# Optimization experiments

Hardware: AMD Instinct MI355X
Metric: run time of the kernel (lower is better)

## Reference

```python
import jax, jax.numpy as jnp
import numpy as np
import math

B, C, H, WIN = 8, 96, 224, 7
D_STATE, DT_RANK = 16, 6
PERK = C // 4
K_RATIO = 0.25


def nearest_perfect_square(val):
    if val <= 0:
        return 0
    s = math.sqrt(val)
    lo = math.floor(s) ** 2
    hi = math.ceil(s) ** 2
    return lo if abs(lo - val) <= abs(hi - val) else hi


def setup_inputs() -> dict:
    key = jax.random.key(0)
    ks = jax.random.split(key, 8)
    x = jax.random.normal(ks[0], (B, C, H, H), dtype=jnp.float32)
    router_w1 = jax.random.normal(ks[1], (C // 4, C), jnp.float32) * (1.0 / math.sqrt(C))
    router_b1 = jnp.zeros((C // 4,), jnp.float32)
    router_w2 = jax.random.normal(ks[2], (1, C // 4), jnp.float32) * (1.0 / math.sqrt(C // 4))
    router_b2 = jnp.zeros((1,), jnp.float32)
    x_proj_weight = jax.random.normal(ks[3], (4, DT_RANK + 2 * D_STATE, PERK), jnp.float32) * (1.0 / math.sqrt(PERK))
    std = DT_RANK ** -0.5
    dt_projs_weight = jax.random.uniform(ks[4], (4, PERK, DT_RANK), jnp.float32, -std, std)
    dt = jnp.exp(jax.random.uniform(ks[5], (4, PERK), jnp.float32) * (math.log(0.1) - math.log(0.001)) + math.log(0.001))
    dt = jnp.clip(dt, 1e-4)
    dt_projs_bias = dt + jnp.log(-jnp.expm1(-dt))  # inv-softplus init as in dt_init_fn
    A_logs = jnp.log(jnp.tile(jnp.arange(1, D_STATE + 1, dtype=jnp.float32)[None, :], (4 * PERK, 1)))
    Ds = jnp.ones((4 * PERK,), jnp.float32)
    return {"x": x, "router_w1": router_w1, "router_b1": router_b1, "router_w2": router_w2,
            "router_b2": router_b2, "x_proj_weight": x_proj_weight, "dt_projs_weight": dt_projs_weight,
            "dt_projs_bias": dt_projs_bias, "A_logs": A_logs, "Ds": Ds}


def reference(x, router_w1, router_b1, router_w2, router_b2, x_proj_weight,
              dt_projs_weight, dt_projs_bias, A_logs, Ds):
    Bb, Cc, Hh, Ww = x.shape
    nH = Hh // WIN
    N = nH * nH
    # window partition: b c (nh p1) (nw p2) -> b (nh nw) c p1 p2
    windows = x.reshape(Bb, Cc, nH, WIN, nH, WIN).transpose(0, 2, 4, 1, 3, 5).reshape(Bb, N, Cc, WIN, WIN)
    # router scores
    pooled = windows.mean(axis=(-2, -1))  # [B,N,C]
    hid = jax.nn.gelu(pooled @ router_w1.T + router_b1, approximate=False)
    logits = (hid @ router_w2.T + router_b2)[..., 0]  # [B,N]
    probs = jax.nn.softmax(logits, axis=1)
    top_k = min(max(nearest_perfect_square(N * K_RATIO), 1), N)
    n = int(math.isqrt(top_k))
    rw, sel = jax.lax.top_k(probs, top_k)  # sorted descending, like torch.topk
    windows_flat = windows.reshape(Bb, N, -1)
    cur = jnp.take_along_axis(windows_flat, sel[:, :, None], axis=1)  # [B,topk,C*w*w]
    cur = cur.reshape(Bb, n, n, Cc, WIN, WIN)
    L = n * n * WIN * WIN
    # channel interleave (p k) -> (k p), k=4
    x_int = cur.reshape(Bb, n, n, Cc // 4, 4, WIN, WIN).transpose(0, 1, 2, 4, 3, 5, 6)  # [B,n,n,4,perK,w,w]

    def local_scan(w, column_first, flip):
        # w: [B,n,n,D,wh,ww] -> [B,D,L]
        if column_first:
            w = w.transpose(0, 3, 2, 1, 5, 4)
        else:
            w = w.transpose(0, 3, 1, 2, 4, 5)
        w = w.reshape(Bb, -1, L)
        if flip:
            w = w[..., ::-1]
        return w

    xs = jnp.stack([
        local_scan(x_int[:, :, :, 0], False, False),
        local_scan(x_int[:, :, :, 1], True, False),
        local_scan(x_int[:, :, :, 2], False, True),
        local_scan(x_int[:, :, :, 3], True, True),
    ], axis=1)  # [B,4,perK,L]

    x_dbl = jnp.einsum('bkdl,kcd->bkcl', xs, x_proj_weight)
    dts = x_dbl[:, :, :DT_RANK]
    Bmat = x_dbl[:, :, DT_RANK:DT_RANK + D_STATE]  # [B,4,Nst,L]
    Cmat = x_dbl[:, :, DT_RANK + D_STATE:]
    dts = jnp.einsum('bkrl,kdr->bkdl', dts, dt_projs_weight)  # [B,4,perK,L]
    A_g = -jnp.exp(A_logs).reshape(4, PERK, D_STATE)
    delta = jax.nn.softplus(dts + dt_projs_bias.reshape(4, PERK)[None, :, :, None])

    # selective scan (grouped): h_{l} = exp(delta*A)*h_{l-1} + delta*u*B_l ; y_l = <h_l, C_l>
    dl = jnp.moveaxis(delta, -1, 0)  # [L,B,4,perK]
    ul = jnp.moveaxis(xs, -1, 0)
    Bl = jnp.moveaxis(Bmat, -1, 0)   # [L,B,4,Nst]
    Cl = jnp.moveaxis(Cmat, -1, 0)
    h0 = jnp.zeros((Bb, 4, PERK, D_STATE), jnp.float32)

    def step(h, inp):
        d, u, Bt, Ct = inp
        h = jnp.exp(d[..., None] * A_g) * h + (d * u)[..., None] * Bt[:, :, None, :]
        return h, jnp.einsum('bkdn,bkn->bkd', h, Ct)

    _, ys = jax.lax.scan(step, h0, (dl, ul, Bl, Cl))
    y = jnp.moveaxis(ys, 0, -1) + xs * Ds.reshape(4, PERK)[None, :, :, None]  # [B,4,perK,L]

    def local_reverse(yk, column_first, flip):
        if flip:
            yk = yk[..., ::-1]
        if column_first:
            yk = yk.reshape(Bb, -1, n, n, WIN, WIN).transpose(0, 1, 3, 5, 2, 4).reshape(Bb, -1, L)
        else:
            yk = yk.reshape(Bb, -1, n, n, WIN, WIN).transpose(0, 1, 2, 4, 3, 5).reshape(Bb, -1, L)
        return yk

    yout = jnp.concatenate([
        local_reverse(y[:, 0], False, False),
        local_reverse(y[:, 1], True, False),
        local_reverse(y[:, 2], False, True),
        local_reverse(y[:, 3], True, True),
    ], axis=1)  # [B,C,L]
    yout = yout.reshape(Bb, Cc, n * n, WIN * WIN).transpose(0, 2, 1, 3).reshape(Bb, top_k, -1)
    cur_out = yout * rw[:, :, None]
    residual = windows_flat * probs[:, :, None]
    residual = residual.at[jnp.arange(Bb)[:, None], sel].set(cur_out)
    new = windows_flat + residual
    return new.reshape(Bb, Cc, -1)
```

## Files before the change

### kernel.cpp

```cpp
#include <hip/hip_runtime.h>
#include <math.h>

#define BBATCH 8
#define CC 96
#define HH 224
#define NHW 32
#define NWIN 1024
#define TOPK 256
#define PERK 24
#define DST 16
#define DTR 6
#define LL 12544
#define LCP 52
#define NG 13
#define TCH 256
#define NBK 32
#define XROW 1248
#define WST2 2912

#define OFF_POOL 0
#define OFF_LOG  786432
#define OFF_PROB 794624
#define OFF_RW   802816
#define OFF_RANK 804864
#define OFF_SEL  813056
#define OFF_WEFF 815104
#define OFF_CP   820480
#define OFF_CS   3966208
#define OFF_XSD  7111936
#define OFF_STG  17335552

#define ROR_ADD(v, CTRL) \
    v += __int_as_float(__builtin_amdgcn_update_dpp(0, __float_as_int(v), CTRL, 0xf, 0xf, true))

__global__ void k_weff(const float* __restrict__ xpw, const float* __restrict__ dtw,
                       float* __restrict__ wcomb) {
    int i = blockIdx.x * blockDim.x + threadIdx.x;
    if (i >= 4 * 56 * PERK) return;
    int k = i / (56 * PERK), rem = i - k * (56 * PERK);
    int row = rem / PERK, c = rem - row * PERK;
    float v;
    if (row < PERK) {
        v = 0.f;
        #pragma unroll
        for (int r = 0; r < DTR; ++r)
            v += dtw[(k * PERK + row) * DTR + r] * xpw[(k * 38 + r) * PERK + c];
    } else {
        v = xpw[(k * 38 + (row - PERK + DTR)) * PERK + c];
    }
    wcomb[i] = v;
}

__global__ void k_pool(const float* __restrict__ x, float* __restrict__ pooled) {
    int bc = blockIdx.x;
    const float* xp = x + (size_t)bc * HH * HH;
    float* pp = pooled + (size_t)bc * NWIN;
    for (int w = threadIdx.x; w < NWIN; w += blockDim.x) {
        int wr = w >> 5, wc = w & 31;
        const float* base = xp + (wr * 7) * HH + wc * 7;
        float s = 0.f;
        #pragma unroll
        for (int i = 0; i < 7; ++i) {
            #pragma unroll
            for (int j = 0; j < 7; ++j) s += base[i * HH + j];
        }
        pp[w] = s * (1.0f / 49.0f);
    }
}

__global__ __launch_bounds__(64) void k_router(
        const float* __restrict__ pooled,
        const float* __restrict__ w1, const float* __restrict__ b1,
        const float* __restrict__ w2, const float* __restrict__ b2,
        float* __restrict__ logits) {
    __shared__ float sw1[PERK * CC];
    __shared__ float sb1[PERK];
    __shared__ float sw2[PERK];
    int b = blockIdx.x >> 4, slice = blockIdx.x & 15;
    int tid = threadIdx.x;
    for (int i = tid; i < PERK * CC; i += 64) sw1[i] = w1[i];
    if (tid < PERK) { sb1[tid] = b1[tid]; sw2[tid] = w2[tid]; }
    __syncthreads();
    int w = slice * 64 + tid;
    float hid[PERK];
    #pragma unroll
    for (int j = 0; j < PERK; ++j) hid[j] = sb1[j];
    const float* pp = pooled + (size_t)b * CC * NWIN + w;
    for (int c = 0; c < CC; ++c) {
        float pv = pp[(size_t)c * NWIN];
        #pragma unroll
        for (int j = 0; j < PERK; ++j) hid[j] += pv * sw1[j * CC + c];
    }
    float lg = b2[0];
    #pragma unroll
    for (int j = 0; j < PERK; ++j) {
        float hv = hid[j];
        float g = 0.5f * hv * (1.0f + erff(hv * 0.7071067811865476f));
        lg += g * sw2[j];
    }
    logits[b * NWIN + w] = lg;
}

__global__ __launch_bounds__(64) void k_rankF(const float* __restrict__ logits,
        float* __restrict__ probs, float* __restrict__ rw,
        int* __restrict__ rank, int* __restrict__ sel) {
    __shared__ __attribute__((aligned(16))) float sp[NWIN];
    __shared__ float red[64];
    int b = blockIdx.x >> 4, slice = blockIdx.x & 15;
    int tid = threadIdx.x;
    for (int i = tid; i < NWIN / 4; i += 64)
        ((float4*)sp)[i] = ((const float4*)(logits + (size_t)b * NWIN))[i];
    __syncthreads();
    float m = -1e30f;
    for (int i = tid; i < NWIN; i += 64) m = fmaxf(m, sp[i]);
    red[tid] = m; __syncthreads();
    for (int o = 32; o > 0; o >>= 1) { if (tid < o) red[tid] = fmaxf(red[tid], red[tid + o]); __syncthreads(); }
    float mx = red[0]; __syncthreads();
    for (int i = tid; i < NWIN; i += 64) sp[i] = expf(sp[i] - mx);
    __syncthreads();
    float s = 0.f;
    for (int i = tid; i < NWIN; i += 64) s += sp[i];
    red[tid] = s; __syncthreads();
    for (int o = 32; o > 0; o >>= 1) { if (tid < o) red[tid] += red[tid + o]; __syncthreads(); }
    float sum = red[0]; __syncthreads();
    for (int i = tid; i < NWIN; i += 64) sp[i] = sp[i] / sum;
    __syncthreads();
    int w = slice * 64 + tid;
    float p = sp[w];
    probs[b * NWIN + w] = p;
    int r = 0;
    for (int j = 0; j < NWIN; j += 4) {
        float4 pj = *(const float4*)&sp[j];
        r += (int)((pj.x > p) || (pj.x == p && (j + 0) < w));
        r += (int)((pj.y > p) || (pj.y == p && (j + 1) < w));
        r += (int)((pj.z > p) || (pj.z == p && (j + 2) < w));
        r += (int)((pj.w > p) || (pj.w == p && (j + 3) < w));
    }
    rank[b * NWIN + w] = r;
    if (r < TOPK) { sel[b * TOPK + r] = w; rw[b * TOPK + r] = p; }
}

__device__ __forceinline__ float softplus_f(float v) {
    return fmaxf(v, 0.f) + __logf(1.0f + __expf(-fabsf(v)));
}

__device__ __forceinline__ int window_wsel(const int* sel, int b, int k, int t) {
    int qscan = (k >= 2) ? (255 - t) : t;
    int selidx = (k & 1) ? (((qscan & 15) << 4) | (qscan >> 4)) : qscan;
    return sel[b * TOPK + selidx];
}

__global__ __launch_bounds__(256) void k_gather(const float* __restrict__ x,
        const int* __restrict__ sel, float* __restrict__ xsd) {
    const int total = NBK * TCH * XROW;
    for (int e = blockIdx.x * 256 + threadIdx.x; e < total; e += gridDim.x * 256) {
        int blk = e / XROW;
        int rem = e - blk * XROW;
        int d2 = rem / LCP, j = rem - d2 * LCP;
        float v = 0.f;
        if (j < 49) {
            int t = blk & 255, bk = blk >> 8, k = bk & 3, b = bk >> 2;
            int wsel = window_wsel(sel, b, k, t);
            int pix = (k >= 2) ? 48 - j : j;
            int q7 = pix / 7, r7 = pix - q7 * 7;
            int wi = (k & 1) ? r7 : q7;
            int wj = (k & 1) ? q7 : r7;
            v = x[(((size_t)b * CC + 4 * d2 + k) * HH + (wsel >> 5) * 7 + wi) * HH
                  + (wsel & 31) * 7 + wj];
        }
        xsd[e] = v;
    }
}

__global__ __launch_bounds__(384, 4) void k_prodD(
        const float* __restrict__ xsd, const float* __restrict__ wcomb,
        const float* __restrict__ dtb, const float* __restrict__ alogs,
        float* __restrict__ stage, float* __restrict__ carrP, float* __restrict__ carrS) {
    __shared__ __attribute__((aligned(16))) float sxs[PERK][LCP];
    __shared__ __attribute__((aligned(16))) float sprj[56][LCP];
    __shared__ float swt[56 * PERK];
    __shared__ float sbias[PERK];
    int blk = blockIdx.x;
    int bk = blk >> 8; int k = bk & 3;
    int tid = threadIdx.x;
    const float4* xin = (const float4*)(xsd + (size_t)blk * XROW);
    for (int i = tid; i < XROW / 4; i += 384) ((float4*)sxs)[i] = xin[i];
    for (int i = tid; i < 56 * PERK; i += 384) swt[i] = wcomb[k * (56 * PERK) + i];
    if (tid < PERK) sbias[tid] = dtb[k * PERK + tid];
    if (tid < 168) {
        int r = tid / 3, j = 49 + tid % 3;
        sprj[r][j] = 0.f;
    }
    int d = tid >> 4, s = tid & 15;
    float A = -__expf(alogs[(k * PERK + d) * DST + s]);
    __syncthreads();
    for (int idx = tid; idx < 56 * NG; idx += 384) {
        int row = idx / NG, g = idx - row * NG; int j = g * 4;
        float bs = (row < PERK) ? sbias[row] : 0.f;
        float ax = bs, ay = bs, az = bs, aw = bs;
        #pragma unroll
        for (int d2 = 0; d2 < PERK; ++d2) {
            float w = swt[row * PERK + d2];
            float4 v = *(const float4*)&sxs[d2][j];
            ax += w * v.x; ay += w * v.y; az += w * v.z; aw += w * v.w;
        }
        if (row < PERK) {
            ax = softplus_f(ax); ay = softplus_f(ay); az = softplus_f(az); aw = softplus_f(aw);
        }
        float* dst = &sprj[row][j];
        if (g < 12) { float4 o = {ax, ay, az, aw}; *(float4*)dst = o; }
        else dst[0] = ax;
    }
    __syncthreads();
    float4* sg = (float4*)(stage + (size_t)blk * WST2);
    const float4* sp4 = (const float4*)&sprj[0][0];
    for (int i = tid; i < WST2 / 4; i += 384) sg[i] = sp4[i];
    float P = 1.f, S = 0.f;
    for (int g = 0; g < NG; ++g) {
        int j = g * 4;
        float4 dl4 = *(const float4*)&sprj[d][j];
        float4 xs4 = *(const float4*)&sxs[d][j];
        float4 B4  = *(const float4*)&sprj[24 + s][j];
        float aa;
        aa = __expf(dl4.x * A); S = aa * S + (dl4.x * xs4.x) * B4.x; P *= aa;
        aa = __expf(dl4.y * A); S = aa * S + (dl4.y * xs4.y) * B4.y; P *= aa;
        aa = __expf(dl4.z * A); S = aa * S + (dl4.z * xs4.z) * B4.z; P *= aa;
        aa = __expf(dl4.w * A); S = aa * S + (dl4.w * xs4.w) * B4.w; P *= aa;
    }
    size_t cidx = (size_t)blk * 384 + tid;
    carrP[cidx] = P; carrS[cidx] = S;
}

__global__ void k_carry(const float* carrP, const float* carrS, float* hin) {
    int gid = blockIdx.x * blockDim.x + threadIdx.x;
    int bk = gid / 384, ds = gid - bk * 384;
    float Hv = 0.f;
    for (int t = 0; t < TCH; ++t) {
        size_t idx = ((size_t)bk * TCH + t) * 384 + ds;
        float pv = carrP[idx], sv = carrS[idx];
        hin[idx] = Hv;
        Hv = pv * Hv + sv;
    }
}

__global__ __launch_bounds__(64) void k_base(const float* __restrict__ x,
        const float* __restrict__ probs, const int* __restrict__ rank,
        float* __restrict__ out) {
    int wr = blockIdx.x % NHW; int bc = blockIdx.x / NHW;
    int b = bc / CC;
    __shared__ float buf[7 * HH];
    __shared__ float fmul[NHW];
    __shared__ int   fsel[NHW];
    int tid = threadIdx.x;
    const float* xp = x + ((size_t)bc * HH + wr * 7) * HH;
    for (int i = tid; i < 7 * HH; i += 64) buf[i] = xp[i];
    if (tid < NHW) {
        int w = wr * NHW + tid;
        fsel[tid] = (rank[b * NWIN + w] < TOPK);
        fmul[tid] = 1.0f + probs[b * NWIN + w];
    }
    __syncthreads();
    int c = bc - b * CC;
    for (int idx = tid; idx < NHW * 49; idx += 64) {
        int wc = idx / 49, r = idx - wc * 49;
        if (fsel[wc]) continue;
        int ri = r / 7, rj = r - ri * 7;
        float v = buf[ri * HH + wc * 7 + rj];
        int w = wr * NHW + wc;
        out[(((size_t)b * NWIN + w) * CC + c) * 49 + r] = v * fmul[wc];
    }
}

__global__ __launch_bounds__(384, 4) void k_scan2(
        const float* __restrict__ alogs, const float* __restrict__ dsv,
        const float* __restrict__ hin, const float* __restrict__ xsd,
        float* __restrict__ stage) {
    __shared__ __attribute__((aligned(16))) float sy[PERK][LCP];
    int blk = blockIdx.x;
    int bk = blk >> 8; int k = bk & 3;
    int tid = threadIdx.x;
    int d = tid >> 4, s = tid & 15;
    float A = -__expf(alogs[(k * PERK + d) * DST + s]);
    float Dsr = dsv[k * PERK + d];
    size_t cidx = (size_t)blk * 384 + tid;
    float h = hin[cidx];
    const float* sg = stage + (size_t)blk * WST2;
    const float* pdl = sg + d * LCP;
    const float* pB  = sg + (24 + s) * LCP;
    const float* pC  = sg + (40 + s) * LCP;
    const float* pxs = xsd + (size_t)blk * XROW + d * LCP;
    float4 dlC = *(const float4*)(pdl);     float4 xsC = *(const float4*)(pxs);
    float4 BC_ = *(const float4*)(pB);      float4 CC_ = *(const float4*)(pC);
    float4 dlN = *(const float4*)(pdl + 4); float4 xsN = *(const float4*)(pxs + 4);
    float4 BN_ = *(const float4*)(pB + 4);  float4 CN_ = *(const float4*)(pC + 4);
    for (int g = 0; g < NG; ++g) {
        float4 dl4 = dlC, xs4 = xsC, B4 = BC_, C4 = CC_;
        dlC = dlN; xsC = xsN; BC_ = BN_; CC_ = CN_;
        if (g + 2 < NG) {
            int jn = (g + 2) * 4;
            dlN = *(const float4*)(pdl + jn); xsN = *(const float4*)(pxs + jn);
            BN_ = *(const float4*)(pB + jn);  CN_ = *(const float4*)(pC + jn);
        }
        int j = g * 4;
        float aa, part;
        aa = __expf(dl4.x * A); h = aa * h + (dl4.x * xs4.x) * B4.x;
        part = h * C4.x;
        ROR_ADD(part, 0x121); ROR_ADD(part, 0x122); ROR_ADD(part, 0x124); ROR_ADD(part, 0x128);
        if (s == 0) sy[d][j] = part + xs4.x * Dsr;
        aa = __expf(dl4.y * A); h = aa * h + (dl4.y * xs4.y) * B4.y;
        part = h * C4.y;
        ROR_ADD(part, 0x121); ROR_ADD(part, 0x122); ROR_ADD(part, 0x124); ROR_ADD(part, 0x128);
        if (s == 0 && j + 1 < 49) sy[d][j + 1] = part + xs4.y * Dsr;
        aa = __expf(dl4.z * A); h = aa * h + (dl4.z * xs4.z) * B4.z;
        part = h * C4.z;
        ROR_ADD(part, 0x121); ROR_ADD(part, 0x122); ROR_ADD(part, 0x124); ROR_ADD(part, 0x128);
        if (s == 0 && j + 2 < 49) sy[d][j + 2] = part + xs4.z * Dsr;
        aa = __expf(dl4.w * A); h = aa * h + (dl4.w * xs4.w) * B4.w;
        part = h * C4.w;
        ROR_ADD(part, 0x121); ROR_ADD(part, 0x122); ROR_ADD(part, 0x124); ROR_ADD(part, 0x128);
        if (s == 0 && j + 3 < 49) sy[d][j + 3] = part + xs4.w * Dsr;
    }
    __syncthreads();
    float* yout = stage + (size_t)blk * WST2;
    for (int idx = tid; idx < PERK * 49; idx += 384) {
        int j = idx / PERK, d2 = idx - j * PERK;
        yout[idx] = sy[d2][j];
    }
}

__global__ __launch_bounds__(256) void k_yadd(const float* __restrict__ stage,
        const float* __restrict__ x, const int* __restrict__ sel,
        const float* __restrict__ rw, float* __restrict__ out) {
    __shared__ float ytile[CC * 49];
    int qo = blockIdx.x & 255; int b = blockIdx.x >> 8;
    int wsel = sel[b * TOPK + qo];
    float p = rw[b * TOPK + qo];
    for (int idx = threadIdx.x; idx < CC * 49; idx += 256) {
        int k = idx / 1176; int r1 = idx - k * 1176;
        int u = r1 / 168;   int r2 = r1 - u * 168;
        int wj = r2 / 24;   int d = r2 - wj * 24;
        int rest = qo * 7 + u;
        int b2 = rest & 15; int aw = rest >> 4;
        int wi = aw % 7;    int a = aw / 7;
        int q   = (k & 1) ? (b2 * 16 + a) : (a * 16 + b2);
        int pix = (k & 1) ? (wj * 7 + wi) : (wi * 7 + wj);
        int uu = q * 49 + pix;
        int l = (k >= 2) ? (LL - 1 - uu) : uu;
        int bk = b * 4 + k;
        int t2 = l / 49, jj = l - t2 * 49;
        ytile[(k * PERK + d) * 49 + u * 7 + wj] =
            p * stage[((size_t)(bk * 256 + t2)) * WST2 + jj * PERK + d];
    }
    __syncthreads();
    float* ob = out + ((size_t)(b * NWIN + wsel) * CC) * 49;
    int gi0 = (wsel >> 5) * 7, gj0 = (wsel & 31) * 7;
    for (int e = threadIdx.x; e < CC * 49; e += 256) {
        int C = e / 49, cell = e - C * 49;
        int u = cell / 7, wj = cell - u * 7;
        float xv = x[(((size_t)b * CC + C) * HH + gi0 + u) * HH + gj0 + wj];
        ob[e] = xv + ytile[e];
    }
}

extern "C" void kernel_launch(void* const* d_in, const int* in_sizes, int n_in,
                              void* d_out, int out_size, void* d_ws, size_t ws_size,
                              hipStream_t stream) {
    const float* x   = (const float*)d_in[0];
    const float* w1  = (const float*)d_in[1];
    const float* b1  = (const float*)d_in[2];
    const float* w2  = (const float*)d_in[3];
    const float* b2  = (const float*)d_in[4];
    const float* xpw = (const float*)d_in[5];
    const float* dtw = (const float*)d_in[6];
    const float* dtb = (const float*)d_in[7];
    const float* alg = (const float*)d_in[8];
    const float* dsv = (const float*)d_in[9];
    float* out = (float*)d_out;
    float* ws  = (float*)d_ws;

    float* pooled = ws + OFF_POOL;
    float* logits = ws + OFF_LOG;
    float* probs  = ws + OFF_PROB;
    float* rwv    = ws + OFF_RW;
    int*   rank   = (int*)(ws + OFF_RANK);
    int*   sel    = (int*)(ws + OFF_SEL);
    float* wcomb  = ws + OFF_WEFF;
    float* cP  = ws + OFF_CP;
    float* cS  = ws + OFF_CS;
    float* xsd = ws + OFF_XSD;
    float* stage = ws + OFF_STG;

    k_pool  <<<BBATCH * CC, 256, 0, stream>>>(x, pooled);
    k_router<<<BBATCH * 16, 64, 0, stream>>>(pooled, w1, b1, w2, b2, logits);
    k_rankF <<<BBATCH * 16, 64, 0, stream>>>(logits, probs, rwv, rank, sel);
    k_weff  <<<(4 * 56 * PERK + 255) / 256, 256, 0, stream>>>(xpw, dtw, wcomb);
    k_gather<<<2048, 256, 0, stream>>>(x, sel, xsd);
    k_prodD <<<NBK * TCH, 384, 0, stream>>>(xsd, wcomb, dtb, alg, stage, cP, cS);
    k_carry <<<48, 256, 0, stream>>>(cP, cS, cP);
    k_base  <<<BBATCH * CC * NHW, 64, 0, stream>>>(x, probs, rank, out);
    k_scan2 <<<NBK * TCH, 384, 0, stream>>>(alg, dsv, cP, xsd, stage);
    k_yadd  <<<BBATCH * TOPK, 256, 0, stream>>>(stage, x, sel, rwv, out);
}
```

Baseline: 487.8 us.

## Interleave scan staging data into packed float4 records for the scan pass

```diff
diff --git a/kernel.cpp b/kernel.cpp
--- a/kernel.cpp
+++ b/kernel.cpp
@@ -17,6 +17,7 @@
 #define NBK 32
 #define XROW 1248
 #define WST2 2912
+#define WST3 4000
 
 #define OFF_POOL 0
 #define OFF_LOG  786432
@@ -29,6 +30,8 @@
 #define OFF_CS   3966208
 #define OFF_XSD  7111936
 #define OFF_STG  17335552
+#define NEED_T   ((size_t)(17335552 + 8192 * WST3) * 4)
+#define NEED_F   ((size_t)(17335552 + 8192 * WST2) * 4)
 
 #define ROR_ADD(v, CTRL) \
     v += __int_as_float(__builtin_amdgcn_update_dpp(0, __float_as_int(v), CTRL, 0xf, 0xf, true))
@@ -172,27 +175,15 @@
     }
 }
 
-__global__ __launch_bounds__(384, 4) void k_prodD(
-        const float* __restrict__ xsd, const float* __restrict__ wcomb,
-        const float* __restrict__ dtb, const float* __restrict__ alogs,
-        float* __restrict__ stage, float* __restrict__ carrP, float* __restrict__ carrS) {
-    __shared__ __attribute__((aligned(16))) float sxs[PERK][LCP];
-    __shared__ __attribute__((aligned(16))) float sprj[56][LCP];
-    __shared__ float swt[56 * PERK];
-    __shared__ float sbias[PERK];
-    int blk = blockIdx.x;
-    int bk = blk >> 8; int k = bk & 3;
-    int tid = threadIdx.x;
+__device__ __forceinline__ void proj_body(
+        float (*sxs)[LCP], float (*sprj)[LCP], float* swt, float* sbias,
+        const float* xsd, const float* wcomb, const float* dtb,
+        int blk, int k, int tid) {
     const float4* xin = (const float4*)(xsd + (size_t)blk * XROW);
     for (int i = tid; i < XROW / 4; i += 384) ((float4*)sxs)[i] = xin[i];
     for (int i = tid; i < 56 * PERK; i += 384) swt[i] = wcomb[k * (56 * PERK) + i];
     if (tid < PERK) sbias[tid] = dtb[k * PERK + tid];
-    if (tid < 168) {
-        int r = tid / 3, j = 49 + tid % 3;
-        sprj[r][j] = 0.f;
-    }
-    int d = tid >> 4, s = tid & 15;
-    float A = -__expf(alogs[(k * PERK + d) * DST + s]);
+    if (tid < 168) { int r = tid / 3, j = 49 + tid % 3; sprj[r][j] = 0.f; }
     __syncthreads();
     for (int idx = tid; idx < 56 * NG; idx += 384) {
         int row = idx / NG, g = idx - row * NG; int j = g * 4;
@@ -212,9 +203,13 @@
         else dst[0] = ax;
     }
     __syncthreads();
-    float4* sg = (float4*)(stage + (size_t)blk * WST2);
-    const float4* sp4 = (const float4*)&sprj[0][0];
-    for (int i = tid; i < WST2 / 4; i += 384) sg[i] = sp4[i];
+}
+
+__device__ __forceinline__ void carry_body(
+        float (*sxs)[LCP], float (*sprj)[LCP], const float* alogs,
+        int blk, int k, int tid, float* carrP, float* carrS) {
+    int d = tid >> 4, s = tid & 15;
+    float A = -__expf(alogs[(k * PERK + d) * DST + s]);
     float P = 1.f, S = 0.f;
     for (int g = 0; g < NG; ++g) {
         int j = g * 4;
@@ -231,6 +226,51 @@
     carrP[cidx] = P; carrS[cidx] = S;
 }
 
+__global__ __launch_bounds__(384, 4) void k_prodT(
+        const float* __restrict__ xsd, const float* __restrict__ wcomb,
+        const float* __restrict__ dtb, const float* __restrict__ alogs,
+        float* __restrict__ stage, float* __restrict__ carrP, float* __restrict__ carrS) {
+    __shared__ __attribute__((aligned(16))) float sxs[PERK][LCP];
+    __shared__ __attribute__((aligned(16))) float sprj[56][LCP];
+    __shared__ float swt[56 * PERK];
+    __shared__ float sbias[PERK];
+    int blk = blockIdx.x; int k = (blk >> 8) & 3;
+    int tid = threadIdx.x;
+    proj_body(sxs, sprj, swt, sbias, xsd, wcomb, dtb, blk, k, tid);
+    float4* sgP = (float4*)(stage + (size_t)blk * WST3);
+    float4* sgQ = sgP + 600;
+    for (int tsk = tid; tsk < 600; tsk += 384) {
+        int jp = tsk / 24, d2 = tsk - jp * 24;
+        int j0 = 2 * jp, j1 = j0 + 1;
+        float4 o = { sprj[d2][j0], sxs[d2][j0], sprj[d2][j1], sxs[d2][j1] };
+        sgP[tsk] = o;
+    }
+    for (int tsk = tid; tsk < 400; tsk += 384) {
+        int jp = tsk / 16, s2 = tsk - jp * 16;
+        int j0 = 2 * jp, j1 = j0 + 1;
+        float4 o = { sprj[24 + s2][j0], sprj[40 + s2][j0], sprj[24 + s2][j1], sprj[40 + s2][j1] };
+        sgQ[tsk] = o;
+    }
+    carry_body(sxs, sprj, alogs, blk, k, tid, carrP, carrS);
+}
+
+__global__ __launch_bounds__(384, 4) void k_prodD(
+        const float* __restrict__ xsd, const float* __restrict__ wcomb,
+        const float* __restrict__ dtb, const float* __restrict__ alogs,
+        float* __restrict__ stage, float* __restrict__ carrP, float* __restrict__ carrS) {
+    __shared__ __attribute__((aligned(16))) float sxs[PERK][LCP];
+    __shared__ __attribute__((aligned(16))) float sprj[56][LCP];
+    __shared__ float swt[56 * PERK];
+    __shared__ float sbias[PERK];
+    int blk = blockIdx.x; int k = (blk >> 8) & 3;
+    int tid = threadIdx.x;
+    proj_body(sxs, sprj, swt, sbias, xsd, wcomb, dtb, blk, k, tid);
+    float4* sg = (float4*)(stage + (size_t)blk * WST2);
+    const float4* sp4 = (const float4*)&sprj[0][0];
+    for (int i = tid; i < WST2 / 4; i += 384) sg[i] = sp4[i];
+    carry_body(sxs, sprj, alogs, blk, k, tid, carrP, carrS);
+}
+
 __global__ void k_carry(const float* carrP, const float* carrS, float* hin) {
     int gid = blockIdx.x * blockDim.x + threadIdx.x;
     int bk = gid / 384, ds = gid - bk * 384;
@@ -271,13 +311,51 @@
     }
 }
 
+__global__ __launch_bounds__(384, 4) void k_scanT(
+        const float* __restrict__ alogs, const float* __restrict__ dsv,
+        const float* __restrict__ hin, const float* __restrict__ stage,
+        float* __restrict__ xsd) {
+    __shared__ __attribute__((aligned(16))) float sy[PERK][LCP];
+    int blk = blockIdx.x; int k = (blk >> 8) & 3;
+    int tid = threadIdx.x;
+    int d = tid >> 4, s = tid & 15;
+    float A = -__expf(alogs[(k * PERK + d) * DST + s]);
+    float Dsr = dsv[k * PERK + d];
+    size_t cidx = (size_t)blk * 384 + tid;
+    float h = hin[cidx];
+    const float4* pP = (const float4*)(stage + (size_t)blk * WST3) + d;
+    const float4* pQ = (const float4*)(stage + (size_t)blk * WST3) + 600 + s;
+    float4 Pc = pP[0],  Qc = pQ[0];
+    float4 Pn = pP[24], Qn = pQ[16];
+    for (int jp = 0; jp < 25; ++jp) {
+        float4 P4 = Pc, Q4 = Qc;
+        Pc = Pn; Qc = Qn;
+        if (jp + 2 < 25) { Pn = pP[(jp + 2) * 24]; Qn = pQ[(jp + 2) * 16]; }
+        int j0 = 2 * jp;
+        float aa, part;
+        aa = __expf(P4.x * A); h = aa * h + (P4.x * P4.y) * Q4.x;
+        part = h * Q4.y;
+        ROR_ADD(part, 0x121); ROR_ADD(part, 0x122); ROR_ADD(part, 0x124); ROR_ADD(part, 0x128);
+        if (s == 0) sy[d][j0] = part + P4.y * Dsr;
+        aa = __expf(P4.z * A); h = aa * h + (P4.z * P4.w) * Q4.z;
+        part = h * Q4.w;
+        ROR_ADD(part, 0x121); ROR_ADD(part, 0x122); ROR_ADD(part, 0x124); ROR_ADD(part, 0x128);
+        if (s == 0 && j0 + 1 < 49) sy[d][j0 + 1] = part + P4.w * Dsr;
+    }
+    __syncthreads();
+    float* yout = xsd + (size_t)blk * XROW;
+    for (int idx = tid; idx < PERK * 49; idx += 384) {
+        int j = idx / PERK, d2 = idx - j * PERK;
+        yout[idx] = sy[d2][j];
+    }
+}
+
 __global__ __launch_bounds__(384, 4) void k_scan2(
         const float* __restrict__ alogs, const float* __restrict__ dsv,
         const float* __restrict__ hin, const float* __restrict__ xsd,
         float* __restrict__ stage) {
     __shared__ __attribute__((aligned(16))) float sy[PERK][LCP];
-    int blk = blockIdx.x;
-    int bk = blk >> 8; int k = bk & 3;
+    int blk = blockIdx.x; int k = (blk >> 8) & 3;
     int tid = threadIdx.x;
     int d = tid >> 4, s = tid & 15;
     float A = -__expf(alogs[(k * PERK + d) * DST + s]);
@@ -328,9 +406,9 @@
     }
 }
 
-__global__ __launch_bounds__(256) void k_yadd(const float* __restrict__ stage,
+__global__ __launch_bounds__(256) void k_yadd(const float* __restrict__ ysrc,
         const float* __restrict__ x, const int* __restrict__ sel,
-        const float* __restrict__ rw, float* __restrict__ out) {
+        const float* __restrict__ rw, float* __restrict__ out, int ystride) {
     __shared__ float ytile[CC * 49];
     int qo = blockIdx.x & 255; int b = blockIdx.x >> 8;
     int wsel = sel[b * TOPK + qo];
@@ -349,7 +427,7 @@
         int bk = b * 4 + k;
         int t2 = l / 49, jj = l - t2 * 49;
         ytile[(k * PERK + d) * 49 + u * 7 + wj] =
-            p * stage[((size_t)(bk * 256 + t2)) * WST2 + jj * PERK + d];
+            p * ysrc[((size_t)(bk * 256 + t2)) * ystride + jj * PERK + d];
     }
     __syncthreads();
     float* ob = out + ((size_t)(b * NWIN + wsel) * CC) * 49;
@@ -395,9 +473,18 @@
     k_rankF <<<BBATCH * 16, 64, 0, stream>>>(logits, probs, rwv, rank, sel);
     k_weff  <<<(4 * 56 * PERK + 255) / 256, 256, 0, stream>>>(xpw, dtw, wcomb);
     k_gather<<<2048, 256, 0, stream>>>(x, sel, xsd);
-    k_prodD <<<NBK * TCH, 384, 0, stream>>>(xsd, wcomb, dtb, alg, stage, cP, cS);
-    k_carry <<<48, 256, 0, stream>>>(cP, cS, cP);
-    k_base  <<<BBATCH * CC * NHW, 64, 0, stream>>>(x, probs, rank, out);
-    k_scan2 <<<NBK * TCH, 384, 0, stream>>>(alg, dsv, cP, xsd, stage);
-    k_yadd  <<<BBATCH * TOPK, 256, 0, stream>>>(stage, x, sel, rwv, out);
-}
+
+    if (ws_size >= NEED_T) {
+        k_prodT<<<NBK * TCH, 384, 0, stream>>>(xsd, wcomb, dtb, alg, stage, cP, cS);
+        k_carry<<<48, 256, 0, stream>>>(cP, cS, cP);
+        k_base <<<BBATCH * CC * NHW, 64, 0, stream>>>(x, probs, rank, out);
+        k_scanT<<<NBK * TCH, 384, 0, stream>>>(alg, dsv, cP, stage, xsd);
+        k_yadd <<<BBATCH * TOPK, 256, 0, stream>>>(xsd, x, sel, rwv, out, XROW);
+    } else {
+        k_prodD<<<NBK * TCH, 384, 0, stream>>>(xsd, wcomb, dtb, alg, stage, cP, cS);
+        k_carry<<<48, 256, 0, stream>>>(cP, cS, cP);
+        k_base <<<BBATCH * CC * NHW, 64, 0, stream>>>(x, probs, rank, out);
+        k_scan2<<<NBK * TCH, 384, 0, stream>>>(alg, dsv, cP, xsd, stage);
+        k_yadd <<<BBATCH * TOPK, 256, 0, stream>>>(stage, x, sel, rwv, out, WST2);
+    }
+}
```

Result: no change. 484.3 us (-0.7%).

## Fuse chunked selective scan into single-pass decoupled look-back kernel

Applied to the files above, without the earlier changes.

```diff
diff --git a/kernel.cpp b/kernel.cpp
--- a/kernel.cpp
+++ b/kernel.cpp
@@ -16,7 +16,6 @@
 #define TCH 256
 #define NBK 32
 #define XROW 1248
-#define WST2 2912
 
 #define OFF_POOL 0
 #define OFF_LOG  786432
@@ -25,10 +24,13 @@
 #define OFF_RANK 804864
 #define OFF_SEL  813056
 #define OFF_WEFF 815104
-#define OFF_CP   820480
-#define OFF_CS   3966208
+#define OFF_PAYA 820480
 #define OFF_XSD  7111936
-#define OFF_STG  17335552
+#define OFF_PAYP 17335552
+#define OFF_FLAG 20481280
+
+#define FLAG_AGG 1
+#define FLAG_PRE 2
 
 #define ROR_ADD(v, CTRL) \
     v += __int_as_float(__builtin_amdgcn_update_dpp(0, __float_as_int(v), CTRL, 0xf, 0xf, true))
@@ -172,27 +174,26 @@
     }
 }
 
-__global__ __launch_bounds__(384, 4) void k_prodD(
-        const float* __restrict__ xsd, const float* __restrict__ wcomb,
+__global__ __launch_bounds__(384, 4) void k_fscan(
+        const float* __restrict__ xsd_in, const float* __restrict__ wcomb,
         const float* __restrict__ dtb, const float* __restrict__ alogs,
-        float* __restrict__ stage, float* __restrict__ carrP, float* __restrict__ carrS) {
+        const float* __restrict__ dsv,
+        unsigned long long* payA, float* payP, int* flags,
+        float* __restrict__ yout_all) {
     __shared__ __attribute__((aligned(16))) float sxs[PERK][LCP];
     __shared__ __attribute__((aligned(16))) float sprj[56][LCP];
+    __shared__ __attribute__((aligned(16))) float sy[PERK][LCP];
     __shared__ float swt[56 * PERK];
     __shared__ float sbias[PERK];
+    __shared__ int sflag;
     int blk = blockIdx.x;
-    int bk = blk >> 8; int k = bk & 3;
+    int t = blk & 255; int k = (blk >> 8) & 3;
     int tid = threadIdx.x;
-    const float4* xin = (const float4*)(xsd + (size_t)blk * XROW);
+    const float4* xin = (const float4*)(xsd_in + (size_t)blk * XROW);
     for (int i = tid; i < XROW / 4; i += 384) ((float4*)sxs)[i] = xin[i];
     for (int i = tid; i < 56 * PERK; i += 384) swt[i] = wcomb[k * (56 * PERK) + i];
     if (tid < PERK) sbias[tid] = dtb[k * PERK + tid];
-    if (tid < 168) {
-        int r = tid / 3, j = 49 + tid % 3;
-        sprj[r][j] = 0.f;
-    }
-    int d = tid >> 4, s = tid & 15;
-    float A = -__expf(alogs[(k * PERK + d) * DST + s]);
+    if (tid < 168) { int r = tid / 3, j = 49 + tid % 3; sprj[r][j] = 0.f; }
     __syncthreads();
     for (int idx = tid; idx < 56 * NG; idx += 384) {
         int row = idx / NG, g = idx - row * NG; int j = g * 4;
@@ -212,9 +213,9 @@
         else dst[0] = ax;
     }
     __syncthreads();
-    float4* sg = (float4*)(stage + (size_t)blk * WST2);
-    const float4* sp4 = (const float4*)&sprj[0][0];
-    for (int i = tid; i < WST2 / 4; i += 384) sg[i] = sp4[i];
+    int d = tid >> 4, s = tid & 15;
+    float A = -__expf(alogs[(k * PERK + d) * DST + s]);
+    float Dsr = dsv[k * PERK + d];
     float P = 1.f, S = 0.f;
     for (int g = 0; g < NG; ++g) {
         int j = g * 4;
@@ -227,81 +228,58 @@
         aa = __expf(dl4.z * A); S = aa * S + (dl4.z * xs4.z) * B4.z; P *= aa;
         aa = __expf(dl4.w * A); S = aa * S + (dl4.w * xs4.w) * B4.w; P *= aa;
     }
-    size_t cidx = (size_t)blk * 384 + tid;
-    carrP[cidx] = P; carrS[cidx] = S;
-}
-
-__global__ void k_carry(const float* carrP, const float* carrS, float* hin) {
-    int gid = blockIdx.x * blockDim.x + threadIdx.x;
-    int bk = gid / 384, ds = gid - bk * 384;
-    float Hv = 0.f;
-    for (int t = 0; t < TCH; ++t) {
-        size_t idx = ((size_t)bk * TCH + t) * 384 + ds;
-        float pv = carrP[idx], sv = carrS[idx];
-        hin[idx] = Hv;
-        Hv = pv * Hv + sv;
-    }
-}
-
-__global__ __launch_bounds__(64) void k_base(const float* __restrict__ x,
-        const float* __restrict__ probs, const int* __restrict__ rank,
-        float* __restrict__ out) {
-    int wr = blockIdx.x % NHW; int bc = blockIdx.x / NHW;
-    int b = bc / CC;
-    __shared__ float buf[7 * HH];
-    __shared__ float fmul[NHW];
-    __shared__ int   fsel[NHW];
-    int tid = threadIdx.x;
-    const float* xp = x + ((size_t)bc * HH + wr * 7) * HH;
-    for (int i = tid; i < 7 * HH; i += 64) buf[i] = xp[i];
-    if (tid < NHW) {
-        int w = wr * NHW + tid;
-        fsel[tid] = (rank[b * NWIN + w] < TOPK);
-        fmul[tid] = 1.0f + probs[b * NWIN + w];
-    }
-    __syncthreads();
-    int c = bc - b * CC;
-    for (int idx = tid; idx < NHW * 49; idx += 64) {
-        int wc = idx / 49, r = idx - wc * 49;
-        if (fsel[wc]) continue;
-        int ri = r / 7, rj = r - ri * 7;
-        float v = buf[ri * HH + wc * 7 + rj];
-        int w = wr * NHW + wc;
-        out[(((size_t)b * NWIN + w) * CC + c) * 49 + r] = v * fmul[wc];
-    }
-}
-
-__global__ __launch_bounds__(384, 4) void k_scan2(
-        const float* __restrict__ alogs, const float* __restrict__ dsv,
-        const float* __restrict__ hin, const float* __restrict__ xsd,
-        float* __restrict__ stage) {
-    __shared__ __attribute__((aligned(16))) float sy[PERK][LCP];
-    int blk = blockIdx.x;
-    int bk = blk >> 8; int k = bk & 3;
-    int tid = threadIdx.x;
-    int d = tid >> 4, s = tid & 15;
-    float A = -__expf(alogs[(k * PERK + d) * DST + s]);
-    float Dsr = dsv[k * PERK + d];
-    size_t cidx = (size_t)blk * 384 + tid;
-    float h = hin[cidx];
-    const float* sg = stage + (size_t)blk * WST2;
-    const float* pdl = sg + d * LCP;
-    const float* pB  = sg + (24 + s) * LCP;
-    const float* pC  = sg + (40 + s) * LCP;
-    const float* pxs = xsd + (size_t)blk * XROW + d * LCP;
-    float4 dlC = *(const float4*)(pdl);     float4 xsC = *(const float4*)(pxs);
-    float4 BC_ = *(const float4*)(pB);      float4 CC_ = *(const float4*)(pC);
-    float4 dlN = *(const float4*)(pdl + 4); float4 xsN = *(const float4*)(pxs + 4);
-    float4 BN_ = *(const float4*)(pB + 4);  float4 CN_ = *(const float4*)(pC + 4);
+    if (t > 0) {
+        unsigned long long w = ((unsigned long long)__float_as_uint(P) << 32) | __float_as_uint(S);
+        __hip_atomic_store(&payA[(size_t)blk * 384 + tid], w,
+                           __ATOMIC_RELAXED, __HIP_MEMORY_SCOPE_AGENT);
+        __syncthreads();
+        if (tid == 0)
+            __hip_atomic_store(&flags[blk], FLAG_AGG, __ATOMIC_RELEASE, __HIP_MEMORY_SCOPE_AGENT);
+    }
+    float h_in = 0.f;
+    if (t > 0) {
+        float accP = 1.f, accS = 0.f;
+        int i = blk - 1;
+        for (;;) {
+            if (tid == 0) {
+                int st;
+                do {
+                    st = __hip_atomic_load(&flags[i], __ATOMIC_ACQUIRE, __HIP_MEMORY_SCOPE_AGENT);
+                    if (st == 0) __builtin_amdgcn_s_sleep(2);
+                } while (st == 0);
+                sflag = st;
+            }
+            __syncthreads();
+            int st = sflag;
+            __syncthreads();
+            if (st == FLAG_PRE) {
+                float hp = __hip_atomic_load(&payP[(size_t)i * 384 + tid],
+                                             __ATOMIC_RELAXED, __HIP_MEMORY_SCOPE_AGENT);
+                h_in = accS + accP * hp;
+                break;
+            } else {
+                unsigned long long w = __hip_atomic_load(&payA[(size_t)i * 384 + tid],
+                                             __ATOMIC_RELAXED, __HIP_MEMORY_SCOPE_AGENT);
+                float Pa = __uint_as_float((unsigned)(w >> 32));
+                float Sa = __uint_as_float((unsigned)(w & 0xffffffffu));
+                accS += accP * Sa; accP *= Pa;
+                --i;
+            }
+        }
+    }
+    float h_out = S + P * h_in;
+    __hip_atomic_store(&payP[(size_t)blk * 384 + tid], h_out,
+                       __ATOMIC_RELAXED, __HIP_MEMORY_SCOPE_AGENT);
+    __syncthreads();
+    if (tid == 0)
+        __hip_atomic_store(&flags[blk], FLAG_PRE, __ATOMIC_RELEASE, __HIP_MEMORY_SCOPE_AGENT);
+    float h = h_in;
     for (int g = 0; g < NG; ++g) {
-        float4 dl4 = dlC, xs4 = xsC, B4 = BC_, C4 = CC_;
-        dlC = dlN; xsC = xsN; BC_ = BN_; CC_ = CN_;
-        if (g + 2 < NG) {
-            int jn = (g + 2) * 4;
-            dlN = *(const float4*)(pdl + jn); xsN = *(const float4*)(pxs + jn);
-            BN_ = *(const float4*)(pB + jn);  CN_ = *(const float4*)(pC + jn);
-        }
         int j = g * 4;
+        float4 dl4 = *(const float4*)&sprj[d][j];
+        float4 xs4 = *(const float4*)&sxs[d][j];
+        float4 B4  = *(const float4*)&sprj[24 + s][j];
+        float4 C4  = *(const float4*)&sprj[40 + s][j];
         float aa, part;
         aa = __expf(dl4.x * A); h = aa * h + (dl4.x * xs4.x) * B4.x;
         part = h * C4.x;
@@ -321,14 +299,42 @@
         if (s == 0 && j + 3 < 49) sy[d][j + 3] = part + xs4.w * Dsr;
     }
     __syncthreads();
-    float* yout = stage + (size_t)blk * WST2;
+    float* yout = yout_all + (size_t)blk * XROW;
     for (int idx = tid; idx < PERK * 49; idx += 384) {
         int j = idx / PERK, d2 = idx - j * PERK;
         yout[idx] = sy[d2][j];
     }
 }
 
-__global__ __launch_bounds__(256) void k_yadd(const float* __restrict__ stage,
+__global__ __launch_bounds__(64) void k_base(const float* __restrict__ x,
+        const float* __restrict__ probs, const int* __restrict__ rank,
+        float* __restrict__ out) {
+    int wr = blockIdx.x % NHW; int bc = blockIdx.x / NHW;
+    int b = bc / CC;
+    __shared__ float buf[7 * HH];
+    __shared__ float fmul[NHW];
+    __shared__ int   fsel[NHW];
+    int tid = threadIdx.x;
+    const float* xp = x + ((size_t)bc * HH + wr * 7) * HH;
+    for (int i = tid; i < 7 * HH; i += 64) buf[i] = xp[i];
+    if (tid < NHW) {
+        int w = wr * NHW + tid;
+        fsel[tid] = (rank[b * NWIN + w] < TOPK);
+        fmul[tid] = 1.0f + probs[b * NWIN + w];
+    }
+    __syncthreads();
+    int c = bc - b * CC;
+    for (int idx = tid; idx < NHW * 49; idx += 64) {
+        int wc = idx / 49, r = idx - wc * 49;
+        if (fsel[wc]) continue;
+        int ri = r / 7, rj = r - ri * 7;
+        float v = buf[ri * HH + wc * 7 + rj];
+        int w = wr * NHW + wc;
+        out[(((size_t)b * NWIN + w) * CC + c) * 49 + r] = v * fmul[wc];
+    }
+}
+
+__global__ __launch_bounds__(256) void k_yadd(const float* __restrict__ ysrc,
         const float* __restrict__ x, const int* __restrict__ sel,
         const float* __restrict__ rw, float* __restrict__ out) {
     __shared__ float ytile[CC * 49];
@@ -349,7 +355,7 @@
         int bk = b * 4 + k;
         int t2 = l / 49, jj = l - t2 * 49;
         ytile[(k * PERK + d) * 49 + u * 7 + wj] =
-            p * stage[((size_t)(bk * 256 + t2)) * WST2 + jj * PERK + d];
+            p * ysrc[((size_t)(bk * 256 + t2)) * XROW + jj * PERK + d];
     }
     __syncthreads();
     float* ob = out + ((size_t)(b * NWIN + wsel) * CC) * 49;
@@ -385,19 +391,19 @@
     int*   rank   = (int*)(ws + OFF_RANK);
     int*   sel    = (int*)(ws + OFF_SEL);
     float* wcomb  = ws + OFF_WEFF;
-    float* cP  = ws + OFF_CP;
-    float* cS  = ws + OFF_CS;
-    float* xsd = ws + OFF_XSD;
-    float* stage = ws + OFF_STG;
-
+    unsigned long long* payA = (unsigned long long*)(ws + OFF_PAYA);
+    float* xsd  = ws + OFF_XSD;
+    float* payP = ws + OFF_PAYP;
+    int*   flags = (int*)(ws + OFF_FLAG);
+
+    hipMemsetAsync(flags, 0, NBK * TCH * sizeof(int), stream);
     k_pool  <<<BBATCH * CC, 256, 0, stream>>>(x, pooled);
     k_router<<<BBATCH * 16, 64, 0, stream>>>(pooled, w1, b1, w2, b2, logits);
     k_rankF <<<BBATCH * 16, 64, 0, stream>>>(logits, probs, rwv, rank, sel);
     k_weff  <<<(4 * 56 * PERK + 255) / 256, 256, 0, stream>>>(xpw, dtw, wcomb);
     k_gather<<<2048, 256, 0, stream>>>(x, sel, xsd);
-    k_prodD <<<NBK * TCH, 384, 0, stream>>>(xsd, wcomb, dtb, alg, stage, cP, cS);
-    k_carry <<<48, 256, 0, stream>>>(cP, cS, cP);
+    k_fscan <<<NBK * TCH, 384, 0, stream>>>(xsd, wcomb, dtb, alg, dsv,
+                                            payA, payP, flags, xsd);
     k_base  <<<BBATCH * CC * NHW, 64, 0, stream>>>(x, probs, rank, out);
-    k_scan2 <<<NBK * TCH, 384, 0, stream>>>(alg, dsv, cP, xsd, stage);
-    k_yadd  <<<BBATCH * TOPK, 256, 0, stream>>>(stage, x, sel, rwv, out);
-}
+    k_yadd  <<<BBATCH * TOPK, 256, 0, stream>>>(xsd, x, sel, rwv, out);
+}
```

Result: slower. 1.718 ms (+252.1%).

## Stage scan inputs as packed bf16 pairs in interleaved layout for scan pass

Applied to the files above, without the earlier changes.

```diff
diff --git a/kernel.cpp b/kernel.cpp
--- a/kernel.cpp
+++ b/kernel.cpp
@@ -16,7 +16,7 @@
 #define TCH 256
 #define NBK 32
 #define XROW 1248
-#define WST2 2912
+#define WST4 2080
 
 #define OFF_POOL 0
 #define OFF_LOG  786432
@@ -32,6 +32,16 @@
 
 #define ROR_ADD(v, CTRL) \
     v += __int_as_float(__builtin_amdgcn_update_dpp(0, __float_as_int(v), CTRL, 0xf, 0xf, true))
+
+__device__ __forceinline__ unsigned f2b(float f) {
+    unsigned u = __float_as_uint(f);
+    return (u + 0x7fffu + ((u >> 16) & 1u)) >> 16;
+}
+__device__ __forceinline__ unsigned pk(float a, float b) {
+    return f2b(a) | (f2b(b) << 16);
+}
+__device__ __forceinline__ float lo_f(unsigned w) { return __uint_as_float(w << 16); }
+__device__ __forceinline__ float hi_f(unsigned w) { return __uint_as_float(w & 0xffff0000u); }
 
 __global__ void k_weff(const float* __restrict__ xpw, const float* __restrict__ dtw,
                        float* __restrict__ wcomb) {
@@ -172,7 +182,7 @@
     }
 }
 
-__global__ __launch_bounds__(384, 4) void k_prodD(
+__global__ __launch_bounds__(384, 4) void k_prodT(
         const float* __restrict__ xsd, const float* __restrict__ wcomb,
         const float* __restrict__ dtb, const float* __restrict__ alogs,
         float* __restrict__ stage, float* __restrict__ carrP, float* __restrict__ carrS) {
@@ -180,19 +190,13 @@
     __shared__ __attribute__((aligned(16))) float sprj[56][LCP];
     __shared__ float swt[56 * PERK];
     __shared__ float sbias[PERK];
-    int blk = blockIdx.x;
-    int bk = blk >> 8; int k = bk & 3;
+    int blk = blockIdx.x; int k = (blk >> 8) & 3;
     int tid = threadIdx.x;
     const float4* xin = (const float4*)(xsd + (size_t)blk * XROW);
     for (int i = tid; i < XROW / 4; i += 384) ((float4*)sxs)[i] = xin[i];
     for (int i = tid; i < 56 * PERK; i += 384) swt[i] = wcomb[k * (56 * PERK) + i];
     if (tid < PERK) sbias[tid] = dtb[k * PERK + tid];
-    if (tid < 168) {
-        int r = tid / 3, j = 49 + tid % 3;
-        sprj[r][j] = 0.f;
-    }
-    int d = tid >> 4, s = tid & 15;
-    float A = -__expf(alogs[(k * PERK + d) * DST + s]);
+    if (tid < 168) { int r = tid / 3, j = 49 + tid % 3; sprj[r][j] = 0.f; }
     __syncthreads();
     for (int idx = tid; idx < 56 * NG; idx += 384) {
         int row = idx / NG, g = idx - row * NG; int j = g * 4;
@@ -212,9 +216,28 @@
         else dst[0] = ax;
     }
     __syncthreads();
-    float4* sg = (float4*)(stage + (size_t)blk * WST2);
-    const float4* sp4 = (const float4*)&sprj[0][0];
-    for (int i = tid; i < WST2 / 4; i += 384) sg[i] = sp4[i];
+    uint4* sgP = (uint4*)(stage + (size_t)blk * WST4);
+    uint4* sgQ = sgP + 312;
+    for (int tsk = tid; tsk < 312; tsk += 384) {
+        int g4 = tsk / 24, d2 = tsk - g4 * 24; int j = g4 * 4;
+        uint4 o;
+        o.x = pk(sprj[d2][j + 0], sxs[d2][j + 0]);
+        o.y = pk(sprj[d2][j + 1], sxs[d2][j + 1]);
+        o.z = pk(sprj[d2][j + 2], sxs[d2][j + 2]);
+        o.w = pk(sprj[d2][j + 3], sxs[d2][j + 3]);
+        sgP[tsk] = o;
+    }
+    for (int tsk = tid; tsk < 208; tsk += 384) {
+        int g4 = tsk / 16, s2 = tsk - g4 * 16; int j = g4 * 4;
+        uint4 o;
+        o.x = pk(sprj[24 + s2][j + 0], sprj[40 + s2][j + 0]);
+        o.y = pk(sprj[24 + s2][j + 1], sprj[40 + s2][j + 1]);
+        o.z = pk(sprj[24 + s2][j + 2], sprj[40 + s2][j + 2]);
+        o.w = pk(sprj[24 + s2][j + 3], sprj[40 + s2][j + 3]);
+        sgQ[tsk] = o;
+    }
+    int d = tid >> 4, s = tid & 15;
+    float A = -__expf(alogs[(k * PERK + d) * DST + s]);
     float P = 1.f, S = 0.f;
     for (int g = 0; g < NG; ++g) {
         int j = g * 4;
@@ -271,64 +294,52 @@
     }
 }
 
-__global__ __launch_bounds__(384, 4) void k_scan2(
+#define BSTEP(pw, qw, jj)                                                          \
+    {                                                                              \
+        float dl_ = lo_f(pw), xs_ = hi_f(pw), Bv_ = lo_f(qw), Cv_ = hi_f(qw);      \
+        float aa_ = __expf(dl_ * A);                                               \
+        h = aa_ * h + (dl_ * xs_) * Bv_;                                           \
+        float part_ = h * Cv_;                                                     \
+        ROR_ADD(part_, 0x121); ROR_ADD(part_, 0x122);                              \
+        ROR_ADD(part_, 0x124); ROR_ADD(part_, 0x128);                              \
+        if (s == 0 && (jj) < 49) sy[d][jj] = part_ + xs_ * Dsr;                    \
+    }
+
+__global__ __launch_bounds__(384, 4) void k_scanT(
         const float* __restrict__ alogs, const float* __restrict__ dsv,
-        const float* __restrict__ hin, const float* __restrict__ xsd,
-        float* __restrict__ stage) {
+        const float* __restrict__ hin, const float* __restrict__ stage,
+        float* __restrict__ xsd) {
     __shared__ __attribute__((aligned(16))) float sy[PERK][LCP];
-    int blk = blockIdx.x;
-    int bk = blk >> 8; int k = bk & 3;
+    int blk = blockIdx.x; int k = (blk >> 8) & 3;
     int tid = threadIdx.x;
     int d = tid >> 4, s = tid & 15;
     float A = -__expf(alogs[(k * PERK + d) * DST + s]);
     float Dsr = dsv[k * PERK + d];
     size_t cidx = (size_t)blk * 384 + tid;
     float h = hin[cidx];
-    const float* sg = stage + (size_t)blk * WST2;
-    const float* pdl = sg + d * LCP;
-    const float* pB  = sg + (24 + s) * LCP;
-    const float* pC  = sg + (40 + s) * LCP;
-    const float* pxs = xsd + (size_t)blk * XROW + d * LCP;
-    float4 dlC = *(const float4*)(pdl);     float4 xsC = *(const float4*)(pxs);
-    float4 BC_ = *(const float4*)(pB);      float4 CC_ = *(const float4*)(pC);
-    float4 dlN = *(const float4*)(pdl + 4); float4 xsN = *(const float4*)(pxs + 4);
-    float4 BN_ = *(const float4*)(pB + 4);  float4 CN_ = *(const float4*)(pC + 4);
-    for (int g = 0; g < NG; ++g) {
-        float4 dl4 = dlC, xs4 = xsC, B4 = BC_, C4 = CC_;
-        dlC = dlN; xsC = xsN; BC_ = BN_; CC_ = CN_;
-        if (g + 2 < NG) {
-            int jn = (g + 2) * 4;
-            dlN = *(const float4*)(pdl + jn); xsN = *(const float4*)(pxs + jn);
-            BN_ = *(const float4*)(pB + jn);  CN_ = *(const float4*)(pC + jn);
-        }
-        int j = g * 4;
-        float aa, part;
-        aa = __expf(dl4.x * A); h = aa * h + (dl4.x * xs4.x) * B4.x;
-        part = h * C4.x;
-        ROR_ADD(part, 0x121); ROR_ADD(part, 0x122); ROR_ADD(part, 0x124); ROR_ADD(part, 0x128);
-        if (s == 0) sy[d][j] = part + xs4.x * Dsr;
-        aa = __expf(dl4.y * A); h = aa * h + (dl4.y * xs4.y) * B4.y;
-        part = h * C4.y;
-        ROR_ADD(part, 0x121); ROR_ADD(part, 0x122); ROR_ADD(part, 0x124); ROR_ADD(part, 0x128);
-        if (s == 0 && j + 1 < 49) sy[d][j + 1] = part + xs4.y * Dsr;
-        aa = __expf(dl4.z * A); h = aa * h + (dl4.z * xs4.z) * B4.z;
-        part = h * C4.z;
-        ROR_ADD(part, 0x121); ROR_ADD(part, 0x122); ROR_ADD(part, 0x124); ROR_ADD(part, 0x128);
-        if (s == 0 && j + 2 < 49) sy[d][j + 2] = part + xs4.z * Dsr;
-        aa = __expf(dl4.w * A); h = aa * h + (dl4.w * xs4.w) * B4.w;
-        part = h * C4.w;
-        ROR_ADD(part, 0x121); ROR_ADD(part, 0x122); ROR_ADD(part, 0x124); ROR_ADD(part, 0x128);
-        if (s == 0 && j + 3 < 49) sy[d][j + 3] = part + xs4.w * Dsr;
-    }
-    __syncthreads();
-    float* yout = stage + (size_t)blk * WST2;
+    const uint4* pP = (const uint4*)(stage + (size_t)blk * WST4) + d;
+    const uint4* pQ = (const uint4*)(stage + (size_t)blk * WST4) + 312 + s;
+    uint4 Pc = pP[0],  Qc = pQ[0];
+    uint4 Pn = pP[24], Qn = pQ[16];
+    for (int g4 = 0; g4 < NG; ++g4) {
+        uint4 P4 = Pc, Q4 = Qc;
+        Pc = Pn; Qc = Qn;
+        if (g4 + 2 < NG) { Pn = pP[(g4 + 2) * 24]; Qn = pQ[(g4 + 2) * 16]; }
+        int j = g4 * 4;
+        BSTEP(P4.x, Q4.x, j);
+        BSTEP(P4.y, Q4.y, j + 1);
+        BSTEP(P4.z, Q4.z, j + 2);
+        BSTEP(P4.w, Q4.w, j + 3);
+    }
+    __syncthreads();
+    float* yout = xsd + (size_t)blk * XROW;
     for (int idx = tid; idx < PERK * 49; idx += 384) {
         int j = idx / PERK, d2 = idx - j * PERK;
         yout[idx] = sy[d2][j];
     }
 }
 
-__global__ __launch_bounds__(256) void k_yadd(const float* __restrict__ stage,
+__global__ __launch_bounds__(256) void k_yadd(const float* __restrict__ ysrc,
         const float* __restrict__ x, const int* __restrict__ sel,
         const float* __restrict__ rw, float* __restrict__ out) {
     __shared__ float ytile[CC * 49];
@@ -349,7 +360,7 @@
         int bk = b * 4 + k;
         int t2 = l / 49, jj = l - t2 * 49;
         ytile[(k * PERK + d) * 49 + u * 7 + wj] =
-            p * stage[((size_t)(bk * 256 + t2)) * WST2 + jj * PERK + d];
+            p * ysrc[((size_t)(bk * 256 + t2)) * XROW + jj * PERK + d];
     }
     __syncthreads();
     float* ob = out + ((size_t)(b * NWIN + wsel) * CC) * 49;
@@ -395,9 +406,9 @@
     k_rankF <<<BBATCH * 16, 64, 0, stream>>>(logits, probs, rwv, rank, sel);
     k_weff  <<<(4 * 56 * PERK + 255) / 256, 256, 0, stream>>>(xpw, dtw, wcomb);
     k_gather<<<2048, 256, 0, stream>>>(x, sel, xsd);
-    k_prodD <<<NBK * TCH, 384, 0, stream>>>(xsd, wcomb, dtb, alg, stage, cP, cS);
+    k_prodT <<<NBK * TCH, 384, 0, stream>>>(xsd, wcomb, dtb, alg, stage, cP, cS);
     k_carry <<<48, 256, 0, stream>>>(cP, cS, cP);
     k_base  <<<BBATCH * CC * NHW, 64, 0, stream>>>(x, probs, rank, out);
-    k_scan2 <<<NBK * TCH, 384, 0, stream>>>(alg, dsv, cP, xsd, stage);
-    k_yadd  <<<BBATCH * TOPK, 256, 0, stream>>>(stage, x, sel, rwv, out);
-}
+    k_scanT <<<NBK * TCH, 384, 0, stream>>>(alg, dsv, cP, stage, xsd);
+    k_yadd  <<<BBATCH * TOPK, 256, 0, stream>>>(xsd, x, sel, rwv, out);
+}
```

Result: faster. 437.2 us (-10.4%).
